# Kernel optimization log

Measured on AMD Instinct MI355X. Metric: run time of the kernel, lower is better.

The kernel has to match this reference:

```python
import jax, jax.numpy as jnp
import numpy as np

H = 64       # HIDDEN_DIM
NH = 2       # attention heads
HD = H // NH # head dim = 32
M = 8        # MEMORY_SLOTS
V = 64       # VOCAB_SIZE


def layer_norm(x, g, b):
    m = x.mean(-1, keepdims=True)
    v = ((x - m) ** 2).mean(-1, keepdims=True)
    return (x - m) / jnp.sqrt(v + 1e-5) * g + b


def mha(x, wi, bi, wo, bo):
    # torch nn.MultiheadAttention, batch_first, self-attention, avg head weights
    B, L, _ = x.shape
    qkv = x @ wi.T + bi                      # (B,L,3H)
    q, k, v = jnp.split(qkv, 3, axis=-1)
    q = q.reshape(B, L, NH, HD)
    k = k.reshape(B, L, NH, HD)
    v = v.reshape(B, L, NH, HD)
    s = jnp.einsum('bqhd,bkhd->bhqk', q, k) / jnp.sqrt(jnp.float32(HD))
    w = jax.nn.softmax(s, axis=-1)           # (B,NH,L,L)
    o = jnp.einsum('bhqk,bkhd->bqhd', w, v).reshape(B, L, H)
    return o @ wo.T + bo, w.mean(axis=1)     # averaged over heads


def ffn(x, w1, b1, w2, b2):
    return jax.nn.relu(x @ w1.T + b1) @ w2.T + b2


def setup_inputs() -> dict:
    key = jax.random.key(0)
    ks = iter(jax.random.split(key, 48))
    p = lambda shape: jax.random.normal(next(ks), shape, jnp.float32) * 0.02
    B, L = 16, 2048
    inp = {
        'seq': jax.random.randint(next(ks), (B, L), 0, V, jnp.int64 if jax.config.jax_enable_x64 else jnp.int32),
        'query': jax.random.randint(next(ks), (B,), 0, V, jnp.int32),
        'target': jax.random.randint(next(ks), (B,), 0, V, jnp.int32),
        'embed': p((V, H)),
        'a1_wi': p((3 * H, H)), 'a1_bi': p((3 * H,)), 'a1_wo': p((H, H)), 'a1_bo': p((H,)),
        'ff1_w1': p((2 * H, H)), 'ff1_b1': p((2 * H,)), 'ff1_w2': p((H, 2 * H)), 'ff1_b2': p((H,)),
        'ln1a_g': jnp.ones((H,)), 'ln1a_b': jnp.zeros((H,)),
        'ln1b_g': jnp.ones((H,)), 'ln1b_b': jnp.zeros((H,)),
        'a2_wi': p((3 * H, H)), 'a2_bi': p((3 * H,)), 'a2_wo': p((H, H)), 'a2_bo': p((H,)),
        'ff2_w1': p((2 * H, H)), 'ff2_b1': p((2 * H,)), 'ff2_w2': p((H, 2 * H)), 'ff2_b2': p((H,)),
        'ln2a_g': jnp.ones((H,)), 'ln2a_b': jnp.zeros((H,)),
        'ln2b_g': jnp.ones((H,)), 'ln2b_b': jnp.zeros((H,)),
        'rq_w': p((H, H)), 'rq_b': p((H,)),
        'ro_w': p((V, H)), 'ro_b': p((V,)),
        'qemb': p((V, H)),
    }
    return inp


def reference(seq, query, target, embed,
              a1_wi, a1_bi, a1_wo, a1_bo, ff1_w1, ff1_b1, ff1_w2, ff1_b2,
              ln1a_g, ln1a_b, ln1b_g, ln1b_b,
              a2_wi, a2_bi, a2_wo, a2_bo, ff2_w1, ff2_b1, ff2_w2, ff2_b2,
              ln2a_g, ln2a_b, ln2b_g, ln2b_b,
              rq_w, rq_b, ro_w, ro_b, qemb):
    # encoder
    h = embed[seq]                                        # (B,L,H)
    a1, _ = mha(h, a1_wi, a1_bi, a1_wo, a1_bo)
    h = layer_norm(h + a1, ln1a_g, ln1a_b)
    h = layer_norm(h + ffn(h, ff1_w1, ff1_b1, ff1_w2, ff1_b2), ln1b_g, ln1b_b)
    a2, attn_w = mha(h, a2_wi, a2_bi, a2_wo, a2_bo)       # attn_w: (B,L,L)
    h = layer_norm(h + a2, ln2a_g, ln2a_b)
    h = layer_norm(h + ffn(h, ff2_w1, ff2_b1, ff2_w2, ff2_b2), ln2b_g, ln2b_b)

    # slot selection (write_mode='attention'): per-key importance, top-k
    importance = attn_w.mean(axis=1)                      # (B,L)
    _, topk = jax.lax.top_k(importance, M)                # (B,M)
    mem = jnp.take_along_axis(h, topk[:, :, None], axis=1)  # (B,M,H)

    # memory reader
    q_h = qemb[query]                                     # (B,H)
    q = q_h @ rq_w.T + rq_b                               # (B,H)
    scores = (q[:, None, :] * mem).sum(-1) / jnp.sqrt(jnp.float32(H))  # (B,M)
    weights = jax.nn.softmax(scores, axis=-1)[:, :, None]
    read = (weights * mem).sum(1)                         # (B,H)
    logits = read @ ro_w.T + ro_b                         # (B,V)

    logp = jax.nn.log_softmax(logits, axis=-1)
    loss = -jnp.mean(logp[jnp.arange(logits.shape[0]), target])
    return loss, attn_w
```

## Files before the change

### kernel.cpp

```cpp
#include <hip/hip_runtime.h>
#include <hip/hip_bf16.h>


typedef unsigned short u16;
#define LQ 2048
#define BBATCH 16
#define QKB 262144

typedef __attribute__((ext_vector_type(8))) short bf16x8;
typedef __attribute__((ext_vector_type(4))) float f32x4;

__device__ __forceinline__ float bfu2f(u16 x){ return __uint_as_float(((unsigned)x) << 16); }
__device__ __forceinline__ u16 f2bu(float f){ return __bfloat16_as_ushort(__float2bfloat16(f)); }

__device__ __forceinline__ const u16* qk_rowp(const u16* qk_r15, const u16* qk_ws,
                                              int bz, int row){
  const u16* base = (bz < 15) ? (qk_r15 + (size_t)bz*QKB) : qk_ws;
  return base + (size_t)row*128;
}
__device__ __forceinline__ u16* qk_rowp_w(u16* qk_r15, u16* qk_ws, int bz, int row){
  u16* base = (bz < 15) ? (qk_r15 + (size_t)bz*QKB) : qk_ws;
  return base + (size_t)row*128;
}

__global__ __launch_bounds__(256) void k_embed(const int* __restrict__ seq,
                                               const float* __restrict__ emb,
                                               u16* __restrict__ h){
  int i = blockIdx.x*256 + threadIdx.x;
  int tok = i >> 6, d = i & 63;
  int v = seq[tok] & 63;
  h[i] = f2bu(emb[(v << 6) + d]);
}

__global__ __launch_bounds__(256) void k_zero(float* __restrict__ p, float* __restrict__ q){
  int i = blockIdx.x*256 + threadIdx.x;
  p[i] = 0.f;
  if (i == 0) q[0] = 0.f;
}

template<int MODE>
__global__ __launch_bounds__(256) void k_qkv(const u16* __restrict__ X,
                                             const float* __restrict__ W,
                                             const float* __restrict__ bias,
                                             u16* __restrict__ dqk0,
                                             u16* __restrict__ dqk_r15,
                                             u16* __restrict__ dqk_ws,
                                             u16* __restrict__ vg){
  __shared__ float WT[64*193];
  __shared__ float bs[192];
  const int t = threadIdx.x;
  for (int e=t; e<192*64; e+=256){ int mo=e>>6, k=e&63; WT[k*193+mo] = W[e]; }
  if (t < 192) bs[t] = bias[t];
  __syncthreads();
  const int wid=t>>6, lane=t&63;
  const int tok0 = (blockIdx.x*4 + wid)*4;
  float x[4];
  #pragma unroll
  for (int c=0;c<4;c++) x[c] = bfu2f(X[(tok0+c)*64 + lane]);
  float acc[4][3];
  #pragma unroll
  for (int c=0;c<4;c++)
    #pragma unroll
    for (int m=0;m<3;m++) acc[c][m] = bs[m*64 + lane];
  for (int k=0;k<64;k++){
    float wv[3];
    #pragma unroll
    for (int m=0;m<3;m++) wv[m] = WT[k*193 + m*64 + lane];
    #pragma unroll
    for (int c=0;c<4;c++){
      float xk = __shfl(x[c], k);
      #pragma unroll
      for (int m=0;m<3;m++) acc[c][m] += xk*wv[m];
    }
  }
  const float qs = 0.17677669529663688f;
  #pragma unroll
  for (int c=0;c<4;c++){
    int tok = tok0+c;
    float vq = acc[c][0]*qs, vk = acc[c][1], vv = acc[c][2];
    int b = tok >> 11, r = tok & 2047;
    u16* row = (MODE==0) ? (dqk0 + (size_t)tok*128) : qk_rowp_w(dqk_r15, dqk_ws, b, r);
    row[lane]      = f2bu(vq);
    row[64 + lane] = f2bu(vk);
    vg[((size_t)((b*64 + (r>>5))*4 + ((r>>2)&3))*64 + lane)*8
       + ((r>>4)&1)*4 + (r&3)] = f2bu(vv);
  }
}

template<int MODE>
__global__ __launch_bounds__(256) void k_attn_ln(const u16* __restrict__ PQK,
    const u16* __restrict__ QKWS, const u16* __restrict__ VG,
    const float* __restrict__ wo, const float* __restrict__ bo,
    const float* __restrict__ g, const float* __restrict__ be,
    u16* __restrict__ h, float* __restrict__ lout){
  __shared__ float OPW[4096];
  __shared__ float ST[16*68];
  __shared__ float DEN[4][2][16];
  __shared__ float LAC[2][16];
  __shared__ float CB[192];
  const int lin = blockIdx.x;
  const int nid = (lin & 7)*256 + (lin >> 3);
  const int qt = nid & 127, bz = nid >> 7;
  const int t = threadIdx.x;
  const int lane = t & 63, wv = t >> 6;
  const int n = lane & 15, gq = lane >> 4;
  const f32x4 FZ = {0.f, 0.f, 0.f, 0.f};

  bf16x8 qf[2];
  {
    const u16* qrow = (MODE==0) ? (PQK + (size_t)(bz*LQ + qt*16 + n)*128)
                                : qk_rowp(PQK, QKWS, bz, qt*16 + n);
    qf[0] = *(const bf16x8*)(qrow + gq*8);
    qf[1] = *(const bf16x8*)(qrow + 32 + gq*8);
  }
  f32x4 o[2][2];
  #pragma unroll
  for (int hh=0; hh<2; hh++)
    #pragma unroll
    for (int db=0; db<2; db++) o[hh][db] = FZ;
  float dacc[2] = {0.f, 0.f};

  #pragma unroll 1
  for (int kt=wv*8; kt<wv*8+8; kt++){
    #pragma unroll
    for (int hh=0; hh<2; hh++){
      f32x4 ev[4];
      #pragma unroll
      for (int jb=0; jb<4; jb++){
        const u16* kr = (MODE==0) ? (PQK + (size_t)(bz*LQ + kt*64 + jb*16 + n)*128)
                                  : qk_rowp(PQK, QKWS, bz, kt*64 + jb*16 + n);
        bf16x8 kf = *(const bf16x8*)(kr + 64 + hh*32 + gq*8);
        ev[jb] = __builtin_amdgcn_mfma_f32_16x16x32_bf16(kf, qf[hh], FZ, 0, 0, 0);
      }
      unsigned pk[4][2];
      float ds = 0.f;
      #pragma unroll
      for (int jb=0; jb<4; jb++){
        float e0 = __expf(ev[jb][0]), e1 = __expf(ev[jb][1]);
        float e2 = __expf(ev[jb][2]), e3 = __expf(ev[jb][3]);
        ds += (e0+e1) + (e2+e3);
        pk[jb][0] = (unsigned)f2bu(e0) | ((unsigned)f2bu(e1) << 16);
        pk[jb][1] = (unsigned)f2bu(e2) | ((unsigned)f2bu(e3) << 16);
      }
      dacc[hh] += ds;
      #pragma unroll
      for (int kb=0; kb<2; kb++){
        union { unsigned u[4]; bf16x8 v; } af;
        af.u[0] = pk[2*kb][0];   af.u[1] = pk[2*kb][1];
        af.u[2] = pk[2*kb+1][0]; af.u[3] = pk[2*kb+1][1];
        #pragma unroll
        for (int db=0; db<2; db++){
          const int d = hh*32 + db*16 + n;
          const bf16x8 vf = *(const bf16x8*)(VG +
              ((size_t)((bz*64 + kt*2 + kb)*4 + gq)*64 + d)*8);
          o[hh][db] = __builtin_amdgcn_mfma_f32_16x16x32_bf16(af.v, vf, o[hh][db], 0, 0, 0);
        }
      }
    }
  }
  #pragma unroll
  for (int hh=0; hh<2; hh++){
    float s = dacc[hh];
    s += __shfl_xor(s, 16);
    s += __shfl_xor(s, 32);
    if (gq == 0) DEN[wv][hh][n] = s;
  }
  #pragma unroll
  for (int hh=0; hh<2; hh++)
    #pragma unroll
    for (int db=0; db<2; db++)
      #pragma unroll
      for (int r=0; r<4; r++)
        OPW[wv*1024 + (gq*4+r)*64 + hh*32 + db*16 + n] = o[hh][db][r];
  __syncthreads();
  if (t < 32){
    int hh = t >> 4, nn = t & 15;
    float s = DEN[0][hh][nn] + DEN[1][hh][nn] + DEN[2][hh][nn] + DEN[3][hh][nn];
    LAC[hh][nn] = s;
    if (lout) lout[(size_t)(bz*2 + hh)*LQ + qt*16 + nn] = s;
  }
  __syncthreads();
  for (int e=t; e<1024; e+=256){
    int q = e >> 6, d = e & 63;
    float s = OPW[e] + OPW[1024+e] + OPW[2048+e] + OPW[3072+e];
    ST[q*68 + d] = s / LAC[d>>5][q];
  }
  __syncthreads();
  float* WOT = OPW;
  for (int e2=t; e2<4096; e2+=256){ int k=e2>>6, mo=e2&63; WOT[e2] = wo[mo*64+k]; }
  if (t < 64)       CB[t] = bo[t];
  else if (t < 128) CB[t] = g[t-64];
  else if (t < 192) CB[t] = be[t-128];
  __syncthreads();
  for (int r=0; r<4; r++){
    int tl = wv*4 + r;
    size_t gtok = (size_t)(bz*LQ + qt*16 + tl);
    float acc = CB[lane];
    for (int k=0; k<64; k++) acc += ST[tl*68 + k] * WOT[k*64 + lane];
    float rr = acc + bfu2f(h[gtok*64 + lane]);
    float s = rr;
    #pragma unroll
    for (int ofs=32; ofs; ofs>>=1) s += __shfl_xor(s, ofs);
    float mean = s * (1.f/64.f);
    float dv = rr - mean;
    float vs = dv*dv;
    #pragma unroll
    for (int ofs=32; ofs; ofs>>=1) vs += __shfl_xor(vs, ofs);
    float rstd = 1.f/sqrtf(vs*(1.f/64.f) + 1e-5f);
    h[gtok*64 + lane] = f2bu(dv*rstd*CB[64+lane] + CB[128+lane]);
  }
}

__global__ __launch_bounds__(256) void k_ffn(u16* __restrict__ h,
    const float* __restrict__ w1, const float* __restrict__ b1,
    const float* __restrict__ w2, const float* __restrict__ b2,
    const float* __restrict__ g, const float* __restrict__ be){
  __shared__ u16 W1L[128*64];
  __shared__ u16 W2L[64*192];
  __shared__ u16 YL[64*64];
  __shared__ float B1[128], B2F[64], G[64], Bb[64];
  const int t = threadIdx.x;
  for (int e=t; e<8192; e+=256){
    int row = e>>6, col = e&63;
    W1L[row*64 + (col ^ ((row&7)<<3))] = f2bu(w1[e]);
  }
  for (int e=t; e<12288; e+=256){
    int o = e/192, rem = e%192, u = rem>>5, gs = rem&31, gq2 = gs>>3, s = gs&7;
    float val;
    if (u < 4) val = w2[o*128 + u*32 + ((s>>2)<<4) + gq2*4 + (s&3)];
    else { int d = ((u-4)<<5) + gq2*8 + s; val = (d==o) ? 1.f : 0.f; }
    W2L[o*192 + ((u*32+gs) ^ ((o&7)<<3))] = f2bu(val);
  }
  if (t < 128) B1[t] = b1[t];
  if (t < 64){ B2F[t] = b2[t]; G[t] = g[t]; Bb[t] = be[t]; }
  __syncthreads();
  const int lane = t & 63, wv = t >> 6;
  const int n = lane & 15, gq = lane >> 4;
  const int tok0 = blockIdx.x*64 + wv*16;
  bf16x8 xf[2];
  xf[0] = *(const bf16x8*)(h + (size_t)(tok0+n)*64 + gq*8);
  xf[1] = *(const bf16x8*)(h + (size_t)(tok0+n)*64 + 32 + gq*8);
  f32x4 acc1[8];
  #pragma unroll
  for (int ct=0; ct<8; ct++){
    f32x4 c;
    #pragma unroll
    for (int r=0;r<4;r++) c[r] = B1[ct*16 + gq*4 + r];
    bf16x8 w1f0 = *(const bf16x8*)(W1L + (ct*16+n)*64 + ((gq*8) ^ ((n&7)<<3)));
    bf16x8 w1f1 = *(const bf16x8*)(W1L + (ct*16+n)*64 + ((32+gq*8) ^ ((n&7)<<3)));
    c = __builtin_amdgcn_mfma_f32_16x16x32_bf16(w1f0, xf[0], c, 0, 0, 0);
    c = __builtin_amdgcn_mfma_f32_16x16x32_bf16(w1f1, xf[1], c, 0, 0, 0);
    acc1[ct] = c;
  }
  f32x4 acc2[4];
  #pragma unroll
  for (int ot=0; ot<4; ot++)
    #pragma unroll
    for (int r=0;r<4;r++) acc2[ot][r] = B2F[ot*16 + gq*4 + r];
  #pragma unroll
  for (int u=0; u<6; u++){
    union { unsigned uu[4]; bf16x8 v; } bfr;
    if (u < 4){
      #pragma unroll
      for (int i=0;i<4;i++){
        int ct = u*2 + (i>>1);
        float a = fmaxf(acc1[ct][(2*i)&3], 0.f);
        float b = fmaxf(acc1[ct][(2*i+1)&3], 0.f);
        bfr.uu[i] = (unsigned)f2bu(a) | ((unsigned)f2bu(b) << 16);
      }
    } else {
      bfr.v = xf[u-4];
    }
    #pragma unroll
    for (int ot=0; ot<4; ot++){
      bf16x8 w2f = *(const bf16x8*)(W2L + (ot*16+n)*192 + ((u*32+gq*8) ^ ((n&7)<<3)));
      acc2[ot] = __builtin_amdgcn_mfma_f32_16x16x32_bf16(w2f, bfr.v, acc2[ot], 0, 0, 0);
    }
  }
  float s1 = 0.f;
  #pragma unroll
  for (int ot=0;ot<4;ot++)
    #pragma unroll
    for (int r=0;r<4;r++) s1 += acc2[ot][r];
  s1 += __shfl_xor(s1, 16); s1 += __shfl_xor(s1, 32);
  float mean = s1 * (1.f/64.f);
  float s2 = 0.f;
  #pragma unroll
  for (int ot=0;ot<4;ot++)
    #pragma unroll
    for (int r=0;r<4;r++){ float dv = acc2[ot][r]-mean; s2 += dv*dv; }
  s2 += __shfl_xor(s2, 16); s2 += __shfl_xor(s2, 32);
  float rstd = 1.f/sqrtf(s2*(1.f/64.f) + 1e-5f);
  #pragma unroll
  for (int ot=0;ot<4;ot++)
    #pragma unroll
    for (int r=0;r<4;r++){
      int o = ot*16 + gq*4 + r;
      float yv = (acc2[ot][r]-mean)*rstd*G[o] + Bb[o];
      YL[(wv*16+n)*64 + (o ^ ((n&7)<<3))] = f2bu(yv);
    }
  __syncthreads();
  unsigned* h32 = (unsigned*)(h + (size_t)(blockIdx.x)*64*64);
  #pragma unroll
  for (int i=0;i<8;i++){
    int idx = i*64 + lane;
    int row = wv*16 + (idx>>5), c32 = idx&31;
    unsigned vv = *(const unsigned*)(YL + row*64 + ((c32*2) ^ ((row&7)<<3)));
    h32[row*32 + c32] = vv;
  }
}

__global__ __launch_bounds__(256) void k_imp(const u16* __restrict__ qk_r15,
    const u16* __restrict__ qk_ws, const float* __restrict__ l2,
    float* __restrict__ imp, int bz0){
  __shared__ float IMPS[2048];
  __shared__ float INVL[128];
  const int t = threadIdx.x;
  const int qt = blockIdx.x, bz = bz0 + blockIdx.y;
  const int lane = t & 63, wv = t >> 6;
  const int n = lane & 15, gq = lane >> 4;
  const f32x4 FZ = {0.f, 0.f, 0.f, 0.f};
  if (t < 128) INVL[t] = 1.f / l2[(size_t)(bz*2 + (t>>6))*LQ + qt*64 + (t&63)];
  for (int e=t; e<2048; e+=256) IMPS[e] = 0.f;
  bf16x8 qf0, qf1;
  {
    const u16* qrow = qk_rowp(qk_r15, qk_ws, bz, qt*64 + wv*16 + n);
    qf0 = *(const bf16x8*)(qrow + gq*8);
    qf1 = *(const bf16x8*)(qrow + 32 + gq*8);
  }
  __syncthreads();
  float iv0[4], iv1[4];
  #pragma unroll
  for (int r=0;r<4;r++){
    iv0[r] = INVL[wv*16 + gq*4 + r];
    iv1[r] = INVL[64 + wv*16 + gq*4 + r];
  }
  for (int kt=0; kt<32; kt++){
    #pragma unroll
    for (int jb=0; jb<4; jb++){
      const u16* kr = qk_rowp(qk_r15, qk_ws, bz, kt*64 + jb*16 + n);
      bf16x8 kf0 = *(const bf16x8*)(kr + 64 + gq*8);
      bf16x8 kf1 = *(const bf16x8*)(kr + 96 + gq*8);
      f32x4 e0 = __builtin_amdgcn_mfma_f32_16x16x32_bf16(qf0, kf0, FZ, 0, 0, 0);
      f32x4 e1 = __builtin_amdgcn_mfma_f32_16x16x32_bf16(qf1, kf1, FZ, 0, 0, 0);
      float cs = 0.f;
      #pragma unroll
      for (int r=0;r<4;r++)
        cs += 0.5f*(__expf(e0[r])*iv0[r] + __expf(e1[r])*iv1[r]);
      cs += __shfl_xor(cs, 16);
      cs += __shfl_xor(cs, 32);
      if (gq == 0) atomicAdd(&IMPS[kt*64 + jb*16 + n], cs);
    }
  }
  __syncthreads();
  for (int e=t; e<2048; e+=256) atomicAdd(&imp[bz*LQ + e], IMPS[e]);
}

template<int DOIMP>
__global__ __launch_bounds__(256) void k_pass2(const u16* __restrict__ qk_r15,
    const u16* __restrict__ qk_ws, const float* __restrict__ l2,
    float* __restrict__ imp, float* __restrict__ wout, int bz0){
  __shared__ float STG[64*68];
  __shared__ float INVL[128];
  const int t = threadIdx.x;
  const int qt = blockIdx.x >> 3, ks = blockIdx.x & 7;
  const int bz = bz0 + blockIdx.y;
  const int lane = t & 63, wv = t >> 6;
  const int n = lane & 15, gq = lane >> 4;
  const f32x4 FZ = {0.f, 0.f, 0.f, 0.f};
  if (t < 128) INVL[t] = 1.f / l2[(size_t)(bz*2 + (t>>6))*LQ + qt*64 + (t&63)];
  bf16x8 qf0, qf1;
  {
    const u16* qrow = qk_rowp(qk_r15, qk_ws, bz, qt*64 + wv*16 + n);
    qf0 = *(const bf16x8*)(qrow + gq*8);
    qf1 = *(const bf16x8*)(qrow + 32 + gq*8);
  }
  __syncthreads();
  const float iv0 = INVL[wv*16 + n], iv1 = INVL[64 + wv*16 + n];
  for (int kt = ks*4; kt < ks*4 + 4; kt++){
    #pragma unroll
    for (int jb=0; jb<4; jb++){
      const u16* kr = qk_rowp(qk_r15, qk_ws, bz, kt*64 + jb*16 + n);
      bf16x8 kf0 = *(const bf16x8*)(kr + 64 + gq*8);
      bf16x8 kf1 = *(const bf16x8*)(kr + 96 + gq*8);
      f32x4 e0 = __builtin_amdgcn_mfma_f32_16x16x32_bf16(kf0, qf0, FZ, 0, 0, 0);
      f32x4 e1 = __builtin_amdgcn_mfma_f32_16x16x32_bf16(kf1, qf1, FZ, 0, 0, 0);
      float4 w4;
      w4.x = 0.5f*(__expf(e0[0])*iv0 + __expf(e1[0])*iv1);
      w4.y = 0.5f*(__expf(e0[1])*iv0 + __expf(e1[1])*iv1);
      w4.z = 0.5f*(__expf(e0[2])*iv0 + __expf(e1[2])*iv1);
      w4.w = 0.5f*(__expf(e0[3])*iv0 + __expf(e1[3])*iv1);
      *(float4*)(&STG[(wv*16 + n)*68 + jb*16 + 4*gq]) = w4;
    }
    size_t base = 1 + (size_t)bz*LQ*LQ + (size_t)(qt*64)*LQ + (size_t)kt*64;
    float p = 0.f;
    for (int r=0; r<16; r++){
      int q = wv*16 + r;
      float v = STG[q*68 + lane];
      wout[base + (size_t)q*LQ + lane] = v;
      p += v;
    }
    if (DOIMP) atomicAdd(&imp[bz*LQ + kt*64 + lane], p);
  }
}

__global__ __launch_bounds__(64) void k_topk(const float* __restrict__ imp,
                                             int* __restrict__ topki){
  __shared__ float v[2048];
  __shared__ float bv[64];
  __shared__ int   bi[64];
  __shared__ int   chosen;
  const int b = blockIdx.x, lane = threadIdx.x;
  for (int i=lane; i<2048; i+=64) v[i] = imp[b*2048 + i];
  __syncthreads();
  for (int m=0; m<8; m++){
    float best = -1e30f; int besti = 1<<30;
    for (int i=lane; i<2048; i+=64)
      if (v[i] > best || (v[i] == best && i < besti)){ best = v[i]; besti = i; }
    bv[lane] = best; bi[lane] = besti;
    __syncthreads();
    if (lane == 0){
      float B = bv[0]; int I = bi[0];
      for (int i2=1; i2<64; i2++)
        if (bv[i2] > B || (bv[i2] == B && bi[i2] < I)){ B = bv[i2]; I = bi[i2]; }
      topki[b*8 + m] = (I < 0) ? 0 : (I > 2047 ? 2047 : I);
      chosen = (I < 0) ? 0 : (I > 2047 ? 2047 : I);
    }
    __syncthreads();
    if (lane == 0) v[chosen] = -1e30f;
    __syncthreads();
  }
}

__global__ __launch_bounds__(64) void k_loss(const u16* __restrict__ h,
    const int* __restrict__ topki, const int* __restrict__ query, const int* __restrict__ target,
    const float* __restrict__ qemb, const float* __restrict__ rq_w, const float* __restrict__ rq_b,
    const float* __restrict__ ro_w, const float* __restrict__ ro_b, float* __restrict__ loss_out){
  const int b = blockIdx.x, lane = threadIdx.x;
  float mv[8];
  #pragma unroll
  for (int m=0; m<8; m++){
    int idx = topki[b*8+m] & 2047;
    mv[m] = bfu2f(h[(size_t)(b*LQ + idx)*64 + lane]);
  }
  float qh = qemb[((query[b]&63)<<6) + lane];
  float qd = rq_b[lane];
  for (int k=0;k<64;k++) qd += __shfl(qh,k) * rq_w[lane*64 + k];
  float sc[8];
  #pragma unroll
  for (int m=0;m<8;m++){
    float p = qd * mv[m];
    #pragma unroll
    for (int o=32;o;o>>=1) p += __shfl_xor(p,o);
    sc[m] = p * 0.125f;
  }
  float mx = sc[0];
  #pragma unroll
  for (int m=1;m<8;m++) mx = fmaxf(mx, sc[m]);
  float den = 0.f, rd = 0.f;
  #pragma unroll
  for (int m=0;m<8;m++){ float w = __expf(sc[m]-mx); den += w; rd += w*mv[m]; }
  rd /= den;
  float lg = ro_b[lane];
  for (int d=0;d<64;d++) lg += __shfl(rd,d) * ro_w[lane*64 + d];
  float lmx = lg;
  #pragma unroll
  for (int o=32;o;o>>=1) lmx = fmaxf(lmx, __shfl_xor(lmx,o));
  float ex = __expf(lg - lmx), es = ex;
  #pragma unroll
  for (int o=32;o;o>>=1) es += __shfl_xor(es,o);
  float lt = __shfl(lg, target[b]&63);
  if (lane == 0) atomicAdd(loss_out, -(lt - lmx - logf(es)) * (1.f/16.f));
}

__global__ void k_store_loss(const float* __restrict__ ls, float* __restrict__ out){
  out[0] = ls[0];
}

extern "C" void kernel_launch(void* const* d_in, const int* in_sizes, int n_in,
                              void* d_out, int out_size, void* d_ws, size_t ws_size,
                              hipStream_t stream){
  const int*   seq    = (const int*)  d_in[0];
  const int*   query  = (const int*)  d_in[1];
  const int*   target = (const int*)  d_in[2];
  const float* embed  = (const float*)d_in[3];
  const float* a1_wi  = (const float*)d_in[4];
  const float* a1_bi  = (const float*)d_in[5];
  const float* a1_wo  = (const float*)d_in[6];
  const float* a1_bo  = (const float*)d_in[7];
  const float* ff1_w1 = (const float*)d_in[8];
  const float* ff1_b1 = (const float*)d_in[9];
  const float* ff1_w2 = (const float*)d_in[10];
  const float* ff1_b2 = (const float*)d_in[11];
  const float* ln1a_g = (const float*)d_in[12];
  const float* ln1a_b = (const float*)d_in[13];
  const float* ln1b_g = (const float*)d_in[14];
  const float* ln1b_b = (const float*)d_in[15];
  const float* a2_wi  = (const float*)d_in[16];
  const float* a2_bi  = (const float*)d_in[17];
  const float* a2_wo  = (const float*)d_in[18];
  const float* a2_bo  = (const float*)d_in[19];
  const float* ff2_w1 = (const float*)d_in[20];
  const float* ff2_b1 = (const float*)d_in[21];
  const float* ff2_w2 = (const float*)d_in[22];
  const float* ff2_b2 = (const float*)d_in[23];
  const float* ln2a_g = (const float*)d_in[24];
  const float* ln2a_b = (const float*)d_in[25];
  const float* ln2b_g = (const float*)d_in[26];
  const float* ln2b_b = (const float*)d_in[27];
  const float* rq_w   = (const float*)d_in[28];
  const float* rq_b   = (const float*)d_in[29];
  const float* ro_w   = (const float*)d_in[30];
  const float* ro_b   = (const float*)d_in[31];
  const float* qemb   = (const float*)d_in[32];

  char* wsb      = (char*)d_ws;
  u16*  qk_ws    = (u16*)(wsb);
  float* ws_imp  = (float*)(wsb + 524288);
  float* ws_l    = (float*)(wsb + 655360);
  int*  ws_top   = (int*)(wsb + 917504);
  float* ws_loss = (float*)(wsb + 918016);

  float* out_f  = (float*)d_out;
  u16* qk1     = (u16*)((char*)d_out + 4194368);
  u16* vg1     = (u16*)((char*)d_out + 12582976);
  u16* vg2     = (u16*)((char*)d_out + 4194368);
  u16* qk_r15  = (u16*)((char*)d_out + 251658304);
  u16* h16     = (u16*)((char*)d_out + 259522624);

  k_embed<<<8192,256,0,stream>>>(seq, embed, h16);
  k_zero<<<128,256,0,stream>>>(ws_imp, ws_loss);
  k_qkv<0><<<2048,256,0,stream>>>(h16, a1_wi, a1_bi, qk1, nullptr, nullptr, vg1);
  k_attn_ln<0><<<2048,256,0,stream>>>(qk1, nullptr, vg1,
                                      a1_wo, a1_bo, ln1a_g, ln1a_b, h16, nullptr);
  k_ffn<<<512,256,0,stream>>>(h16, ff1_w1, ff1_b1, ff1_w2, ff1_b2, ln1b_g, ln1b_b);
  k_qkv<1><<<2048,256,0,stream>>>(h16, a2_wi, a2_bi, nullptr, qk_r15, qk_ws, vg2);
  k_attn_ln<1><<<2048,256,0,stream>>>(qk_r15, qk_ws, vg2,
                                      a2_wo, a2_bo, ln2a_g, ln2a_b, h16, ws_l);
  k_ffn<<<512,256,0,stream>>>(h16, ff2_w1, ff2_b1, ff2_w2, ff2_b2, ln2b_g, ln2b_b);
  k_pass2<1><<<dim3(256,15),256,0,stream>>>(qk_r15, qk_ws, ws_l, ws_imp, out_f, 0);
  k_imp<<<dim3(32,1),256,0,stream>>>(qk_r15, qk_ws, ws_l, ws_imp, 15);
  k_topk<<<16,64,0,stream>>>(ws_imp, ws_top);
  k_loss<<<16,64,0,stream>>>(h16, ws_top, query, target, qemb, rq_w, rq_b, ro_w, ro_b, ws_loss);
  k_pass2<0><<<dim3(256,1),256,0,stream>>>(qk_r15, qk_ws, ws_l, nullptr, out_f, 15);
  k_store_loss<<<1,1,0,stream>>>(ws_loss, out_f);
}
```

Measured before the change: 862.5 us.

## Widen attention query tiles, split k_imp over keys, fuse topk with loss

The attention+LN kernel now handles 32 queries per block instead of 16, so each K fragment load feeds two QK MFMAs and each V fragment feeds two PV MFMAs. Partial outputs and denominators are combined in shared memory with atomics rather than per-wave buffers, and exp results are packed to bf16 with a native packed-convert instruction. k_imp is split across 8 key chunks (256 blocks instead of 32) to expose more parallelism, and k_pass2 uses a swizzled 1D grid. Top-k and loss are fused into one kernel that writes the loss directly, which removes two launches. The risks are LDS atomic contention, higher register pressure under the new launch bound, and more global atomics on the importance array.

```diff
diff --git a/kernel.cpp b/kernel.cpp
--- a/kernel.cpp
+++ b/kernel.cpp
@@ -12,6 +12,12 @@
 
 __device__ __forceinline__ float bfu2f(u16 x){ return __uint_as_float(((unsigned)x) << 16); }
 __device__ __forceinline__ u16 f2bu(float f){ return __bfloat16_as_ushort(__float2bfloat16(f)); }
+
+__device__ __forceinline__ unsigned cvtpk(float lo, float hi){
+  unsigned r;
+  asm("v_cvt_pk_bf16_f32 %0, %1, %2" : "=v"(r) : "v"(lo), "v"(hi));
+  return r;
+}
 
 __device__ __forceinline__ const u16* qk_rowp(const u16* qk_r15, const u16* qk_ws,
                                               int bz, int row){
@@ -88,115 +94,129 @@
 }
 
 template<int MODE>
-__global__ __launch_bounds__(256) void k_attn_ln(const u16* __restrict__ PQK,
+__global__ __launch_bounds__(256, 4) void k_attn_ln(const u16* __restrict__ PQK,
     const u16* __restrict__ QKWS, const u16* __restrict__ VG,
     const float* __restrict__ wo, const float* __restrict__ bo,
     const float* __restrict__ g, const float* __restrict__ be,
     u16* __restrict__ h, float* __restrict__ lout){
-  __shared__ float OPW[4096];
-  __shared__ float ST[16*68];
-  __shared__ float DEN[4][2][16];
-  __shared__ float LAC[2][16];
+  __shared__ float R[4096];
+  __shared__ float ST[32*68];
+  __shared__ float DN[2][32];
   __shared__ float CB[192];
   const int lin = blockIdx.x;
-  const int nid = (lin & 7)*256 + (lin >> 3);
-  const int qt = nid & 127, bz = nid >> 7;
+  const int nid = (lin & 7)*128 + (lin >> 3);
+  const int qt = nid & 63, bz = nid >> 6;
   const int t = threadIdx.x;
   const int lane = t & 63, wv = t >> 6;
   const int n = lane & 15, gq = lane >> 4;
   const f32x4 FZ = {0.f, 0.f, 0.f, 0.f};
 
-  bf16x8 qf[2];
-  {
-    const u16* qrow = (MODE==0) ? (PQK + (size_t)(bz*LQ + qt*16 + n)*128)
-                                : qk_rowp(PQK, QKWS, bz, qt*16 + n);
-    qf[0] = *(const bf16x8*)(qrow + gq*8);
-    qf[1] = *(const bf16x8*)(qrow + 32 + gq*8);
-  }
-  f32x4 o[2][2];
-  #pragma unroll
-  for (int hh=0; hh<2; hh++)
-    #pragma unroll
-    for (int db=0; db<2; db++) o[hh][db] = FZ;
-  float dacc[2] = {0.f, 0.f};
+  for (int e=t; e<2048; e+=256) R[e] = 0.f;
+  if (t < 64) DN[t>>5][t&31] = 0.f;
+  __syncthreads();
+
+  bf16x8 qf[2][2];
+  #pragma unroll
+  for (int qa=0; qa<2; qa++){
+    const u16* qrow = (MODE==0) ? (PQK + (size_t)(bz*LQ + qt*32 + qa*16 + n)*128)
+                                : qk_rowp(PQK, QKWS, bz, qt*32 + qa*16 + n);
+    qf[qa][0] = *(const bf16x8*)(qrow + gq*8);
+    qf[qa][1] = *(const bf16x8*)(qrow + 32 + gq*8);
+  }
+  f32x4 o[2][2][2];
+  #pragma unroll
+  for (int qa=0; qa<2; qa++)
+    #pragma unroll
+    for (int hh=0; hh<2; hh++)
+      #pragma unroll
+      for (int db=0; db<2; db++) o[qa][hh][db] = FZ;
+  float dacc[2][2] = {{0.f,0.f},{0.f,0.f}};
 
   #pragma unroll 1
   for (int kt=wv*8; kt<wv*8+8; kt++){
     #pragma unroll
     for (int hh=0; hh<2; hh++){
-      f32x4 ev[4];
+      bf16x8 kf[4];
       #pragma unroll
       for (int jb=0; jb<4; jb++){
         const u16* kr = (MODE==0) ? (PQK + (size_t)(bz*LQ + kt*64 + jb*16 + n)*128)
                                   : qk_rowp(PQK, QKWS, bz, kt*64 + jb*16 + n);
-        bf16x8 kf = *(const bf16x8*)(kr + 64 + hh*32 + gq*8);
-        ev[jb] = __builtin_amdgcn_mfma_f32_16x16x32_bf16(kf, qf[hh], FZ, 0, 0, 0);
+        kf[jb] = *(const bf16x8*)(kr + 64 + hh*32 + gq*8);
       }
-      unsigned pk[4][2];
-      float ds = 0.f;
-      #pragma unroll
-      for (int jb=0; jb<4; jb++){
-        float e0 = __expf(ev[jb][0]), e1 = __expf(ev[jb][1]);
-        float e2 = __expf(ev[jb][2]), e3 = __expf(ev[jb][3]);
-        ds += (e0+e1) + (e2+e3);
-        pk[jb][0] = (unsigned)f2bu(e0) | ((unsigned)f2bu(e1) << 16);
-        pk[jb][1] = (unsigned)f2bu(e2) | ((unsigned)f2bu(e3) << 16);
+      unsigned pk[2][4][2];
+      #pragma unroll
+      for (int qa=0; qa<2; qa++){
+        f32x4 ev[4];
+        #pragma unroll
+        for (int jb=0; jb<4; jb++)
+          ev[jb] = __builtin_amdgcn_mfma_f32_16x16x32_bf16(kf[jb], qf[qa][hh], FZ, 0, 0, 0);
+        float ds = 0.f;
+        #pragma unroll
+        for (int jb=0; jb<4; jb++){
+          float e0 = __expf(ev[jb][0]), e1 = __expf(ev[jb][1]);
+          float e2 = __expf(ev[jb][2]), e3 = __expf(ev[jb][3]);
+          ds += (e0+e1) + (e2+e3);
+          pk[qa][jb][0] = cvtpk(e0, e1);
+          pk[qa][jb][1] = cvtpk(e2, e3);
+        }
+        dacc[qa][hh] += ds;
       }
-      dacc[hh] += ds;
       #pragma unroll
       for (int kb=0; kb<2; kb++){
-        union { unsigned u[4]; bf16x8 v; } af;
-        af.u[0] = pk[2*kb][0];   af.u[1] = pk[2*kb][1];
-        af.u[2] = pk[2*kb+1][0]; af.u[3] = pk[2*kb+1][1];
+        union { unsigned u[4]; bf16x8 v; } af[2];
+        #pragma unroll
+        for (int qa=0; qa<2; qa++){
+          af[qa].u[0] = pk[qa][2*kb][0];   af[qa].u[1] = pk[qa][2*kb][1];
+          af[qa].u[2] = pk[qa][2*kb+1][0]; af[qa].u[3] = pk[qa][2*kb+1][1];
+        }
         #pragma unroll
         for (int db=0; db<2; db++){
           const int d = hh*32 + db*16 + n;
           const bf16x8 vf = *(const bf16x8*)(VG +
               ((size_t)((bz*64 + kt*2 + kb)*4 + gq)*64 + d)*8);
-          o[hh][db] = __builtin_amdgcn_mfma_f32_16x16x32_bf16(af.v, vf, o[hh][db], 0, 0, 0);
+          #pragma unroll
+          for (int qa=0; qa<2; qa++)
+            o[qa][hh][db] = __builtin_amdgcn_mfma_f32_16x16x32_bf16(af[qa].v, vf, o[qa][hh][db], 0, 0, 0);
         }
       }
     }
   }
   #pragma unroll
-  for (int hh=0; hh<2; hh++){
-    float s = dacc[hh];
-    s += __shfl_xor(s, 16);
-    s += __shfl_xor(s, 32);
-    if (gq == 0) DEN[wv][hh][n] = s;
-  }
-  #pragma unroll
-  for (int hh=0; hh<2; hh++)
-    #pragma unroll
-    for (int db=0; db<2; db++)
-      #pragma unroll
-      for (int r=0; r<4; r++)
-        OPW[wv*1024 + (gq*4+r)*64 + hh*32 + db*16 + n] = o[hh][db][r];
-  __syncthreads();
-  if (t < 32){
-    int hh = t >> 4, nn = t & 15;
-    float s = DEN[0][hh][nn] + DEN[1][hh][nn] + DEN[2][hh][nn] + DEN[3][hh][nn];
-    LAC[hh][nn] = s;
-    if (lout) lout[(size_t)(bz*2 + hh)*LQ + qt*16 + nn] = s;
-  }
-  __syncthreads();
-  for (int e=t; e<1024; e+=256){
+  for (int qa=0; qa<2; qa++)
+    #pragma unroll
+    for (int hh=0; hh<2; hh++){
+      float s = dacc[qa][hh];
+      s += __shfl_xor(s, 16);
+      s += __shfl_xor(s, 32);
+      if (gq == 0) atomicAdd(&DN[hh][qa*16 + n], s);
+    }
+  #pragma unroll
+  for (int qa=0; qa<2; qa++)
+    #pragma unroll
+    for (int hh=0; hh<2; hh++)
+      #pragma unroll
+      for (int db=0; db<2; db++)
+        #pragma unroll
+        for (int r=0; r<4; r++)
+          atomicAdd(&R[(qa*16 + gq*4 + r)*64 + hh*32 + db*16 + n], o[qa][hh][db][r]);
+  __syncthreads();
+  if (lout && t < 64)
+    lout[(size_t)(bz*2 + (t>>5))*LQ + qt*32 + (t&31)] = DN[t>>5][t&31];
+  for (int e=t; e<2048; e+=256){
     int q = e >> 6, d = e & 63;
-    float s = OPW[e] + OPW[1024+e] + OPW[2048+e] + OPW[3072+e];
-    ST[q*68 + d] = s / LAC[d>>5][q];
-  }
-  __syncthreads();
-  float* WOT = OPW;
-  for (int e2=t; e2<4096; e2+=256){ int k=e2>>6, mo=e2&63; WOT[e2] = wo[mo*64+k]; }
+    ST[q*68 + d] = R[e] / DN[d>>5][q];
+  }
+  __syncthreads();
+  for (int e2=t; e2<4096; e2+=256){ int k=e2>>6, mo=e2&63; R[e2] = wo[mo*64+k]; }
   if (t < 64)       CB[t] = bo[t];
   else if (t < 128) CB[t] = g[t-64];
   else if (t < 192) CB[t] = be[t-128];
   __syncthreads();
-  for (int r=0; r<4; r++){
-    int tl = wv*4 + r;
-    size_t gtok = (size_t)(bz*LQ + qt*16 + tl);
+  for (int r=0; r<8; r++){
+    int tl = wv*8 + r;
+    size_t gtok = (size_t)(bz*LQ + qt*32 + tl);
     float acc = CB[lane];
-    for (int k=0; k<64; k++) acc += ST[tl*68 + k] * WOT[k*64 + lane];
+    for (int k=0; k<64; k++) acc += ST[tl*68 + k] * R[k*64 + lane];
     float rr = acc + bfu2f(h[gtok*64 + lane]);
     float s = rr;
     #pragma unroll
@@ -313,15 +333,16 @@
 __global__ __launch_bounds__(256) void k_imp(const u16* __restrict__ qk_r15,
     const u16* __restrict__ qk_ws, const float* __restrict__ l2,
     float* __restrict__ imp, int bz0){
-  __shared__ float IMPS[2048];
+  __shared__ float IMPS[256];
   __shared__ float INVL[128];
   const int t = threadIdx.x;
-  const int qt = blockIdx.x, bz = bz0 + blockIdx.y;
+  const int qt = blockIdx.x >> 3, ks = blockIdx.x & 7;
+  const int bz = bz0;
   const int lane = t & 63, wv = t >> 6;
   const int n = lane & 15, gq = lane >> 4;
   const f32x4 FZ = {0.f, 0.f, 0.f, 0.f};
   if (t < 128) INVL[t] = 1.f / l2[(size_t)(bz*2 + (t>>6))*LQ + qt*64 + (t&63)];
-  for (int e=t; e<2048; e+=256) IMPS[e] = 0.f;
+  IMPS[t] = 0.f;
   bf16x8 qf0, qf1;
   {
     const u16* qrow = qk_rowp(qk_r15, qk_ws, bz, qt*64 + wv*16 + n);
@@ -335,7 +356,7 @@
     iv0[r] = INVL[wv*16 + gq*4 + r];
     iv1[r] = INVL[64 + wv*16 + gq*4 + r];
   }
-  for (int kt=0; kt<32; kt++){
+  for (int kt=ks*4; kt<ks*4+4; kt++){
     #pragma unroll
     for (int jb=0; jb<4; jb++){
       const u16* kr = qk_rowp(qk_r15, qk_ws, bz, kt*64 + jb*16 + n);
@@ -349,22 +370,25 @@
         cs += 0.5f*(__expf(e0[r])*iv0[r] + __expf(e1[r])*iv1[r]);
       cs += __shfl_xor(cs, 16);
       cs += __shfl_xor(cs, 32);
-      if (gq == 0) atomicAdd(&IMPS[kt*64 + jb*16 + n], cs);
-    }
-  }
-  __syncthreads();
-  for (int e=t; e<2048; e+=256) atomicAdd(&imp[bz*LQ + e], IMPS[e]);
+      if (gq == 0) atomicAdd(&IMPS[(kt-ks*4)*64 + jb*16 + n], cs);
+    }
+  }
+  __syncthreads();
+  atomicAdd(&imp[bz*LQ + ks*256 + t], IMPS[t]);
 }
 
 template<int DOIMP>
 __global__ __launch_bounds__(256) void k_pass2(const u16* __restrict__ qk_r15,
     const u16* __restrict__ qk_ws, const float* __restrict__ l2,
-    float* __restrict__ imp, float* __restrict__ wout, int bz0){
+    float* __restrict__ imp, float* __restrict__ wout, int bz0, int nper){
   __shared__ float STG[64*68];
   __shared__ float INVL[128];
+  const int x = blockIdx.x;
+  const int nid = (x & 7)*nper + (x >> 3);
+  const int bz = bz0 + (nid >> 8);
+  const int rem = nid & 255;
+  const int qt = rem >> 3, ks = rem & 7;
   const int t = threadIdx.x;
-  const int qt = blockIdx.x >> 3, ks = blockIdx.x & 7;
-  const int bz = bz0 + blockIdx.y;
   const int lane = t & 63, wv = t >> 6;
   const int n = lane & 15, gq = lane >> 4;
   const f32x4 FZ = {0.f, 0.f, 0.f, 0.f};
@@ -404,12 +428,16 @@
   }
 }
 
-__global__ __launch_bounds__(64) void k_topk(const float* __restrict__ imp,
-                                             int* __restrict__ topki){
+__global__ __launch_bounds__(64) void k_select(const float* __restrict__ imp,
+    const u16* __restrict__ h,
+    const int* __restrict__ query, const int* __restrict__ target,
+    const float* __restrict__ qemb, const float* __restrict__ rq_w, const float* __restrict__ rq_b,
+    const float* __restrict__ ro_w, const float* __restrict__ ro_b, float* __restrict__ out0){
   __shared__ float v[2048];
   __shared__ float bv[64];
   __shared__ int   bi[64];
   __shared__ int   chosen;
+  __shared__ int   topi[8];
   const int b = blockIdx.x, lane = threadIdx.x;
   for (int i=lane; i<2048; i+=64) v[i] = imp[b*2048 + i];
   __syncthreads();
@@ -423,24 +451,18 @@
       float B = bv[0]; int I = bi[0];
       for (int i2=1; i2<64; i2++)
         if (bv[i2] > B || (bv[i2] == B && bi[i2] < I)){ B = bv[i2]; I = bi[i2]; }
-      topki[b*8 + m] = (I < 0) ? 0 : (I > 2047 ? 2047 : I);
-      chosen = (I < 0) ? 0 : (I > 2047 ? 2047 : I);
+      int c = (I < 0) ? 0 : (I > 2047 ? 2047 : I);
+      topi[m] = c;
+      chosen = c;
     }
     __syncthreads();
     if (lane == 0) v[chosen] = -1e30f;
     __syncthreads();
   }
-}
-
-__global__ __launch_bounds__(64) void k_loss(const u16* __restrict__ h,
-    const int* __restrict__ topki, const int* __restrict__ query, const int* __restrict__ target,
-    const float* __restrict__ qemb, const float* __restrict__ rq_w, const float* __restrict__ rq_b,
-    const float* __restrict__ ro_w, const float* __restrict__ ro_b, float* __restrict__ loss_out){
-  const int b = blockIdx.x, lane = threadIdx.x;
   float mv[8];
   #pragma unroll
   for (int m=0; m<8; m++){
-    int idx = topki[b*8+m] & 2047;
+    int idx = topi[m] & 2047;
     mv[m] = bfu2f(h[(size_t)(b*LQ + idx)*64 + lane]);
   }
   float qh = qemb[((query[b]&63)<<6) + lane];
@@ -470,11 +492,7 @@
   #pragma unroll
   for (int o=32;o;o>>=1) es += __shfl_xor(es,o);
   float lt = __shfl(lg, target[b]&63);
-  if (lane == 0) atomicAdd(loss_out, -(lt - lmx - logf(es)) * (1.f/16.f));
-}
-
-__global__ void k_store_loss(const float* __restrict__ ls, float* __restrict__ out){
-  out[0] = ls[0];
+  if (lane == 0) atomicAdd(out0, -(lt - lmx - logf(es)) * (1.f/16.f));
 }
 
 extern "C" void kernel_launch(void* const* d_in, const int* in_sizes, int n_in,
@@ -518,8 +536,6 @@
   u16*  qk_ws    = (u16*)(wsb);
   float* ws_imp  = (float*)(wsb + 524288);
   float* ws_l    = (float*)(wsb + 655360);
-  int*  ws_top   = (int*)(wsb + 917504);
-  float* ws_loss = (float*)(wsb + 918016);
 
   float* out_f  = (float*)d_out;
   u16* qk1     = (u16*)((char*)d_out + 4194368);
@@ -529,19 +545,18 @@
   u16* h16     = (u16*)((char*)d_out + 259522624);
 
   k_embed<<<8192,256,0,stream>>>(seq, embed, h16);
-  k_zero<<<128,256,0,stream>>>(ws_imp, ws_loss);
+  k_zero<<<128,256,0,stream>>>(ws_imp, out_f);
   k_qkv<0><<<2048,256,0,stream>>>(h16, a1_wi, a1_bi, qk1, nullptr, nullptr, vg1);
-  k_attn_ln<0><<<2048,256,0,stream>>>(qk1, nullptr, vg1,
+  k_attn_ln<0><<<1024,256,0,stream>>>(qk1, nullptr, vg1,
                                       a1_wo, a1_bo, ln1a_g, ln1a_b, h16, nullptr);
   k_ffn<<<512,256,0,stream>>>(h16, ff1_w1, ff1_b1, ff1_w2, ff1_b2, ln1b_g, ln1b_b);
   k_qkv<1><<<2048,256,0,stream>>>(h16, a2_wi, a2_bi, nullptr, qk_r15, qk_ws, vg2);
-  k_attn_ln<1><<<2048,256,0,stream>>>(qk_r15, qk_ws, vg2,
+  k_attn_ln<1><<<1024,256,0,stream>>>(qk_r15, qk_ws, vg2,
                                       a2_wo, a2_bo, ln2a_g, ln2a_b, h16, ws_l);
   k_ffn<<<512,256,0,stream>>>(h16, ff2_w1, ff2_b1, ff2_w2, ff2_b2, ln2b_g, ln2b_b);
-  k_pass2<1><<<dim3(256,15),256,0,stream>>>(qk_r15, qk_ws, ws_l, ws_imp, out_f, 0);
-  k_imp<<<dim3(32,1),256,0,stream>>>(qk_r15, qk_ws, ws_l, ws_imp, 15);
-  k_topk<<<16,64,0,stream>>>(ws_imp, ws_top);
-  k_loss<<<16,64,0,stream>>>(h16, ws_top, query, target, qemb, rq_w, rq_b, ro_w, ro_b, ws_loss);
-  k_pass2<0><<<dim3(256,1),256,0,stream>>>(qk_r15, qk_ws, ws_l, nullptr, out_f, 15);
-  k_store_loss<<<1,1,0,stream>>>(ws_loss, out_f);
-}
+  k_pass2<1><<<3840,256,0,stream>>>(qk_r15, qk_ws, ws_l, ws_imp, out_f, 0, 480);
+  k_imp<<<256,256,0,stream>>>(qk_r15, qk_ws, ws_l, ws_imp, 15);
+  k_select<<<16,64,0,stream>>>(ws_imp, h16, query, target, qemb,
+                               rq_w, rq_b, ro_w, ro_b, out_f);
+  k_pass2<0><<<256,256,0,stream>>>(qk_r15, qk_ws, ws_l, nullptr, out_f, 15, 32);
+}
```

New measurement: 838.1 us. -2.8%, faster.
